# Optimization experiments

Measured on AMD Instinct MI355X. Metric: run time of the kernel, lower is better.

The kernel has to match this reference:

```python
import jax, jax.numpy as jnp
import numpy as np

N = 200_000          # instances (patches) in the bag
D = 512              # dim_compress_features
NCLS = 2             # n_class
NINS = 8             # n_ins (top-k per polarity)


def setup_inputs() -> dict:
    key = jax.random.key(0)
    k1, k2, k3 = jax.random.split(key, 3)
    return {
        "bag_label": 1,
        "h": jax.random.normal(k1, (N, D), dtype=jnp.float32),
        "A": jax.random.normal(k2, (N, 1, NCLS), dtype=jnp.float32),
        # Dense(n_class) params of the (shared) instance classifier
        "W": jax.random.normal(k3, (D, NCLS), dtype=jnp.float32) * 0.02,
        "b": jnp.zeros((NCLS,), dtype=jnp.float32),
    }


def reference(bag_label, h, A, W, b):
    # Attention scores for the bag's class: A[j][0][bag_label]  -> [N]
    A_I = A[:, 0, bag_label]
    # top n_ins most-attended (positive evidence) and least-attended (negative)
    _, pos_idx = jax.lax.top_k(A_I, NINS)    # [NINS]
    _, neg_idx = jax.lax.top_k(-A_I, NINS)   # [NINS]
    idx = jnp.concatenate([pos_idx, neg_idx], axis=0)   # [2*NINS]
    ins_in = h[idx]                                      # gather -> [2*NINS, D]
    # Batched Dense + softmax (replaces the per-instance Python loop)
    logits_unnorm = ins_in @ W + b                       # [2*NINS, NCLS]
    logits = jax.nn.softmax(logits_unnorm, axis=-1)      # [2*NINS, NCLS]
    ins_labels = jnp.concatenate(
        [jnp.full((NINS,), 1, dtype=jnp.int32), jnp.full((NINS,), 0, dtype=jnp.int32)]
    )
    return ins_labels, logits_unnorm, logits
```

## Files before the change

kernel.cpp:

```cpp
#include <hip/hip_runtime.h>
#include <math.h>

#define N_ELEMS 200000
#define D 512
#define NCLS 2
#define NINS 8
#define NBLK1 128
#define NTHR1 512
#define NTHR2 1024

typedef unsigned long long u64;
typedef unsigned int u32;

__device__ __forceinline__ u32 mono(float f) {
    u32 u = __float_as_uint(f);
    return u ^ (u32)(((int)u >> 31) | 0x80000000);
}

__device__ __forceinline__ u64 make_key(float v, int i) {
    return ((u64)mono(v) << 32) | (u32)(~(u32)i);
}
__device__ __forceinline__ int key_idx(u64 k) { return (int)(~(u32)k); }

__device__ __forceinline__ u64 shfl_xor_u64(u64 x, int m) {
    u32 lo = (u32)x, hi = (u32)(x >> 32);
    lo = __shfl_xor(lo, m, 64);
    hi = __shfl_xor(hi, m, 64);
    return ((u64)hi << 32) | lo;
}

__device__ __forceinline__ u64 wave_max_u64(u64 k) {
#pragma unroll
    for (int m = 1; m < 64; m <<= 1) {
        u64 o = shfl_xor_u64(k, m);
        if (o > k) k = o;
    }
    return k;
}

__global__ __launch_bounds__(NTHR1) void scan_partial(const int* __restrict__ bl_ptr,
                                                      const float* __restrict__ A,
                                                      u64* __restrict__ wsTop,
                                                      u64* __restrict__ wsBot) {
    const int tid  = threadIdx.x;
    const int blk  = blockIdx.x;
    const int wid  = tid >> 6;
    const int lane = tid & 63;
    const int bl   = bl_ptr[0];

    __shared__ u64 cand[2][8][NINS];

    const int chunk = (N_ELEMS + NBLK1 - 1) / NBLK1;
    const int start = blk * chunk;
    const int end   = min(N_ELEMS, start + chunk);
    const float2* A2 = (const float2*)A;

    u64 t0, t1, t2, t3, b0, b1, b2, b3;
    {
        int i0 = start + tid, i1 = i0 + NTHR1, i2 = i1 + NTHR1, i3 = i2 + NTHR1;
        float2 a;
        if (i0 < end) { a = A2[i0]; float v = bl ? a.y : a.x; t0 = make_key(v, i0); b0 = make_key(-v, i0); } else { t0 = b0 = 0; }
        if (i1 < end) { a = A2[i1]; float v = bl ? a.y : a.x; t1 = make_key(v, i1); b1 = make_key(-v, i1); } else { t1 = b1 = 0; }
        if (i2 < end) { a = A2[i2]; float v = bl ? a.y : a.x; t2 = make_key(v, i2); b2 = make_key(-v, i2); } else { t2 = b2 = 0; }
        if (i3 < end) { a = A2[i3]; float v = bl ? a.y : a.x; t3 = make_key(v, i3); b3 = make_key(-v, i3); } else { t3 = b3 = 0; }
    }

#pragma unroll
    for (int r = 0; r < NINS; ++r) {
        u64 m01 = t0 > t1 ? t0 : t1;
        u64 m23 = t2 > t3 ? t2 : t3;
        u64 lm  = m01 > m23 ? m01 : m23;
        u64 w   = wave_max_u64(lm);
        if (lane == 0) cand[0][wid][r] = w;
        if (t0 == w) t0 = 0; if (t1 == w) t1 = 0; if (t2 == w) t2 = 0; if (t3 == w) t3 = 0;
    }
#pragma unroll
    for (int r = 0; r < NINS; ++r) {
        u64 m01 = b0 > b1 ? b0 : b1;
        u64 m23 = b2 > b3 ? b2 : b3;
        u64 lm  = m01 > m23 ? m01 : m23;
        u64 w   = wave_max_u64(lm);
        if (lane == 0) cand[1][wid][r] = w;
        if (b0 == w) b0 = 0; if (b1 == w) b1 = 0; if (b2 == w) b2 = 0; if (b3 == w) b3 = 0;
    }
    __syncthreads();

    if (wid < 2) {
        u64 k = cand[wid][lane >> 3][lane & 7];
        u64 mine = 0;
#pragma unroll
        for (int r = 0; r < NINS; ++r) {
            u64 w = wave_max_u64(k);
            if (lane == r) mine = w;
            if (k == w) k = 0;
        }
        u64* dst = (wid == 0) ? wsTop : wsBot;
        if (lane < NINS) dst[blk * NINS + lane] = mine;
    }
}

__global__ __launch_bounds__(NTHR2) void finalize(const float* __restrict__ h,
                                                  const float* __restrict__ W,
                                                  const float* __restrict__ bvec,
                                                  const u64* __restrict__ wsTop,
                                                  const u64* __restrict__ wsBot,
                                                  float* __restrict__ out) {
    const int tid  = threadIdx.x;
    const int wid  = tid >> 6;
    const int lane = tid & 63;

    __shared__ u64 cand2[16][NINS];
    __shared__ int fidx[2 * NINS];

    {
        const u64* src = (wid < 8) ? wsTop : wsBot;
        const int base = (wid & 7) * 128;
        u64 ka = src[base + lane];
        u64 kb = src[base + 64 + lane];
        u64 mine = 0;
#pragma unroll
        for (int r = 0; r < NINS; ++r) {
            u64 m_ = ka > kb ? ka : kb;
            u64 w  = wave_max_u64(m_);
            if (lane == r) mine = w;
            if (ka == w) ka = 0;
            if (kb == w) kb = 0;
        }
        if (lane < NINS) cand2[wid][lane] = mine;
    }
    __syncthreads();

    if ((wid & 7) == 0) {
        const u64* flat = &cand2[(wid >> 3) * 8][0];
        u64 k = flat[lane];
        int got = 0;
#pragma unroll
        for (int r = 0; r < NINS; ++r) {
            u64 w = wave_max_u64(k);
            if (lane == r) got = key_idx(w);
            if (k == w) k = 0;
        }
        if (lane < NINS) fidx[(wid >> 3) * NINS + lane] = got;
    }
    __syncthreads();

    const long long row = fidx[wid];
    const float4* h4 = (const float4*)(h + row * (long long)D);
    const float2* W2 = (const float2*)W;

    float s0 = 0.f, s1 = 0.f;
#pragma unroll
    for (int it = 0; it < 2; ++it) {
        int d4 = lane + it * 64;
        float4 x = h4[d4];
        float2 w0 = W2[d4 * 4 + 0];
        float2 w1 = W2[d4 * 4 + 1];
        float2 w2 = W2[d4 * 4 + 2];
        float2 w3 = W2[d4 * 4 + 3];
        s0 += x.x * w0.x + x.y * w1.x + x.z * w2.x + x.w * w3.x;
        s1 += x.x * w0.y + x.y * w1.y + x.z * w2.y + x.w * w3.y;
    }
#pragma unroll
    for (int m = 1; m < 64; m <<= 1) {
        s0 += __shfl_xor(s0, m, 64);
        s1 += __shfl_xor(s1, m, 64);
    }
    if (lane == 0) {
        float l0 = s0 + bvec[0];
        float l1 = s1 + bvec[1];
        float mx = fmaxf(l0, l1);
        float e0 = expf(l0 - mx), e1 = expf(l1 - mx);
        float inv = 1.0f / (e0 + e1);
        out[16 + wid * 2 + 0] = l0;
        out[16 + wid * 2 + 1] = l1;
        out[48 + wid * 2 + 0] = e0 * inv;
        out[48 + wid * 2 + 1] = e1 * inv;
    }
    if (tid < 16) out[tid] = (tid < 8) ? 1.0f : 0.0f;
}

extern "C" void kernel_launch(void* const* d_in, const int* in_sizes, int n_in,
                              void* d_out, int out_size, void* d_ws, size_t ws_size,
                              hipStream_t stream) {
    const int*   bl = (const int*)  d_in[0];
    const float* h  = (const float*)d_in[1];
    const float* A  = (const float*)d_in[2];
    const float* W  = (const float*)d_in[3];
    const float* b  = (const float*)d_in[4];
    float* out = (float*)d_out;

    char* ws = (char*)d_ws;
    u64* wsTop = (u64*)(ws + 0);
    u64* wsBot = (u64*)(ws + 8192);

    scan_partial<<<NBLK1, NTHR1, 0, stream>>>(bl, A, wsTop, wsBot);
    finalize<<<1, NTHR2, 0, stream>>>(h, W, b, wsTop, wsBot, out);
}
```

Baseline: 25.27 us.

## Fuse scan and finalize into one cooperative kernel with grid sync

Merges the partial top-k scan and the final reduction/gather/dense into a single cooperative kernel that uses a grid-wide barrier instead of a second kernel launch. The finalize phase is reworked for 512 threads: each wave reduces four candidates per lane and computes two output rows. This targets the launch gap between the two small kernels, but cooperative launch plus grid sync carries its own overhead. If cooperative launch fails, it falls back to the two-kernel path.

```diff
diff --git a/kernel.cpp b/kernel.cpp
--- a/kernel.cpp
+++ b/kernel.cpp
@@ -1,13 +1,15 @@
 #include <hip/hip_runtime.h>
+#include <hip/hip_cooperative_groups.h>
 #include <math.h>
+
+namespace cg = cooperative_groups;
 
 #define N_ELEMS 200000
 #define D 512
 #define NCLS 2
 #define NINS 8
-#define NBLK1 128
-#define NTHR1 512
-#define NTHR2 1024
+#define NBLK 128
+#define NTHR 512
 
 typedef unsigned long long u64;
 typedef unsigned int u32;
@@ -38,26 +40,18 @@
     return k;
 }
 
-__global__ __launch_bounds__(NTHR1) void scan_partial(const int* __restrict__ bl_ptr,
-                                                      const float* __restrict__ A,
-                                                      u64* __restrict__ wsTop,
-                                                      u64* __restrict__ wsBot) {
-    const int tid  = threadIdx.x;
-    const int blk  = blockIdx.x;
-    const int wid  = tid >> 6;
-    const int lane = tid & 63;
-    const int bl   = bl_ptr[0];
-
-    __shared__ u64 cand[2][8][NINS];
-
-    const int chunk = (N_ELEMS + NBLK1 - 1) / NBLK1;
+__device__ __forceinline__ void scan_phase(int blk, int tid, int wid, int lane, int bl,
+                                           const float* __restrict__ A,
+                                           u64* __restrict__ wsTop, u64* __restrict__ wsBot,
+                                           u64 (*cand)[8][NINS]) {
+    const int chunk = (N_ELEMS + NBLK - 1) / NBLK;
     const int start = blk * chunk;
     const int end   = min(N_ELEMS, start + chunk);
     const float2* A2 = (const float2*)A;
 
     u64 t0, t1, t2, t3, b0, b1, b2, b3;
     {
-        int i0 = start + tid, i1 = i0 + NTHR1, i2 = i1 + NTHR1, i3 = i2 + NTHR1;
+        int i0 = start + tid, i1 = i0 + NTHR, i2 = i1 + NTHR, i3 = i2 + NTHR;
         float2 a;
         if (i0 < end) { a = A2[i0]; float v = bl ? a.y : a.x; t0 = make_key(v, i0); b0 = make_key(-v, i0); } else { t0 = b0 = 0; }
         if (i1 < end) { a = A2[i1]; float v = bl ? a.y : a.x; t1 = make_key(v, i1); b1 = make_key(-v, i1); } else { t1 = b1 = 0; }
@@ -99,40 +93,34 @@
     }
 }
 
-__global__ __launch_bounds__(NTHR2) void finalize(const float* __restrict__ h,
-                                                  const float* __restrict__ W,
-                                                  const float* __restrict__ bvec,
-                                                  const u64* __restrict__ wsTop,
-                                                  const u64* __restrict__ wsBot,
-                                                  float* __restrict__ out) {
-    const int tid  = threadIdx.x;
-    const int wid  = tid >> 6;
-    const int lane = tid & 63;
-
-    __shared__ u64 cand2[16][NINS];
-    __shared__ int fidx[2 * NINS];
-
+__device__ __forceinline__ void final_phase(int tid, int wid, int lane,
+                                            const float* __restrict__ h,
+                                            const float* __restrict__ W,
+                                            const float* __restrict__ bvec,
+                                            const u64* __restrict__ wsTop,
+                                            const u64* __restrict__ wsBot,
+                                            float* __restrict__ out,
+                                            u64 (*cand2)[NINS], int* fidx) {
     {
-        const u64* src = (wid < 8) ? wsTop : wsBot;
-        const int base = (wid & 7) * 128;
-        u64 ka = src[base + lane];
-        u64 kb = src[base + 64 + lane];
+        const u64* src = (wid < 4) ? wsTop : wsBot;
+        const int base = (wid & 3) * 256 + lane;
+        u64 k0 = src[base], k1 = src[base + 64], k2 = src[base + 128], k3 = src[base + 192];
         u64 mine = 0;
 #pragma unroll
         for (int r = 0; r < NINS; ++r) {
-            u64 m_ = ka > kb ? ka : kb;
-            u64 w  = wave_max_u64(m_);
+            u64 m01 = k0 > k1 ? k0 : k1;
+            u64 m23 = k2 > k3 ? k2 : k3;
+            u64 lm  = m01 > m23 ? m01 : m23;
+            u64 w   = wave_max_u64(lm);
             if (lane == r) mine = w;
-            if (ka == w) ka = 0;
-            if (kb == w) kb = 0;
+            if (k0 == w) k0 = 0; if (k1 == w) k1 = 0; if (k2 == w) k2 = 0; if (k3 == w) k3 = 0;
         }
         if (lane < NINS) cand2[wid][lane] = mine;
     }
     __syncthreads();
 
-    if ((wid & 7) == 0) {
-        const u64* flat = &cand2[(wid >> 3) * 8][0];
-        u64 k = flat[lane];
+    if ((wid & 3) == 0) {
+        u64 k = (lane < 32) ? cand2[(wid & 4) + (lane >> 3)][lane & 7] : 0ULL;
         int got = 0;
 #pragma unroll
         for (int r = 0; r < NINS; ++r) {
@@ -140,43 +128,91 @@
             if (lane == r) got = key_idx(w);
             if (k == w) k = 0;
         }
-        if (lane < NINS) fidx[(wid >> 3) * NINS + lane] = got;
+        if (lane < NINS) fidx[(wid >> 2) * NINS + lane] = got;
     }
     __syncthreads();
 
-    const long long row = fidx[wid];
-    const float4* h4 = (const float4*)(h + row * (long long)D);
     const float2* W2 = (const float2*)W;
-
-    float s0 = 0.f, s1 = 0.f;
-#pragma unroll
-    for (int it = 0; it < 2; ++it) {
-        int d4 = lane + it * 64;
-        float4 x = h4[d4];
-        float2 w0 = W2[d4 * 4 + 0];
-        float2 w1 = W2[d4 * 4 + 1];
-        float2 w2 = W2[d4 * 4 + 2];
-        float2 w3 = W2[d4 * 4 + 3];
-        s0 += x.x * w0.x + x.y * w1.x + x.z * w2.x + x.w * w3.x;
-        s1 += x.x * w0.y + x.y * w1.y + x.z * w2.y + x.w * w3.y;
-    }
-#pragma unroll
-    for (int m = 1; m < 64; m <<= 1) {
-        s0 += __shfl_xor(s0, m, 64);
-        s1 += __shfl_xor(s1, m, 64);
-    }
-    if (lane == 0) {
-        float l0 = s0 + bvec[0];
-        float l1 = s1 + bvec[1];
-        float mx = fmaxf(l0, l1);
-        float e0 = expf(l0 - mx), e1 = expf(l1 - mx);
-        float inv = 1.0f / (e0 + e1);
-        out[16 + wid * 2 + 0] = l0;
-        out[16 + wid * 2 + 1] = l1;
-        out[48 + wid * 2 + 0] = e0 * inv;
-        out[48 + wid * 2 + 1] = e1 * inv;
+#pragma unroll
+    for (int rr = 0; rr < 2; ++rr) {
+        const int g = wid + rr * 8;
+        const long long row = fidx[g];
+        const float4* h4 = (const float4*)(h + row * (long long)D);
+        float s0 = 0.f, s1 = 0.f;
+#pragma unroll
+        for (int it = 0; it < 2; ++it) {
+            int d4 = lane + it * 64;
+            float4 x = h4[d4];
+            float2 w0 = W2[d4 * 4 + 0];
+            float2 w1 = W2[d4 * 4 + 1];
+            float2 w2 = W2[d4 * 4 + 2];
+            float2 w3 = W2[d4 * 4 + 3];
+            s0 += x.x * w0.x + x.y * w1.x + x.z * w2.x + x.w * w3.x;
+            s1 += x.x * w0.y + x.y * w1.y + x.z * w2.y + x.w * w3.y;
+        }
+#pragma unroll
+        for (int m = 1; m < 64; m <<= 1) {
+            s0 += __shfl_xor(s0, m, 64);
+            s1 += __shfl_xor(s1, m, 64);
+        }
+        if (lane == 0) {
+            float l0 = s0 + bvec[0];
+            float l1 = s1 + bvec[1];
+            float mx = fmaxf(l0, l1);
+            float e0 = expf(l0 - mx), e1 = expf(l1 - mx);
+            float inv = 1.0f / (e0 + e1);
+            out[16 + g * 2 + 0] = l0;
+            out[16 + g * 2 + 1] = l1;
+            out[48 + g * 2 + 0] = e0 * inv;
+            out[48 + g * 2 + 1] = e1 * inv;
+        }
     }
     if (tid < 16) out[tid] = (tid < 8) ? 1.0f : 0.0f;
+}
+
+__global__ __launch_bounds__(NTHR) void ins_coop(const int* __restrict__ bl_ptr,
+                                                 const float* __restrict__ A,
+                                                 const float* __restrict__ h,
+                                                 const float* __restrict__ W,
+                                                 const float* __restrict__ bvec,
+                                                 u64* __restrict__ wsTop,
+                                                 u64* __restrict__ wsBot,
+                                                 float* __restrict__ out) {
+    const int tid  = threadIdx.x;
+    const int wid  = tid >> 6;
+    const int lane = tid & 63;
+
+    __shared__ u64 cand[2][8][NINS];
+    __shared__ u64 cand2[8][NINS];
+    __shared__ int fidx[16];
+
+    scan_phase(blockIdx.x, tid, wid, lane, bl_ptr[0], A, wsTop, wsBot, cand);
+
+    cg::this_grid().sync();
+    if (blockIdx.x != 0) return;
+
+    final_phase(tid, wid, lane, h, W, bvec, wsTop, wsBot, out, cand2, fidx);
+}
+
+__global__ __launch_bounds__(NTHR) void scan_partial(const int* __restrict__ bl_ptr,
+                                                     const float* __restrict__ A,
+                                                     u64* __restrict__ wsTop,
+                                                     u64* __restrict__ wsBot) {
+    __shared__ u64 cand[2][8][NINS];
+    scan_phase(blockIdx.x, threadIdx.x, threadIdx.x >> 6, threadIdx.x & 63,
+               bl_ptr[0], A, wsTop, wsBot, cand);
+}
+
+__global__ __launch_bounds__(NTHR) void finalize(const float* __restrict__ h,
+                                                 const float* __restrict__ W,
+                                                 const float* __restrict__ bvec,
+                                                 const u64* __restrict__ wsTop,
+                                                 const u64* __restrict__ wsBot,
+                                                 float* __restrict__ out) {
+    __shared__ u64 cand2[8][NINS];
+    __shared__ int fidx[16];
+    final_phase(threadIdx.x, threadIdx.x >> 6, threadIdx.x & 63,
+                h, W, bvec, wsTop, wsBot, out, cand2, fidx);
 }
 
 extern "C" void kernel_launch(void* const* d_in, const int* in_sizes, int n_in,
@@ -193,6 +229,12 @@
     u64* wsTop = (u64*)(ws + 0);
     u64* wsBot = (u64*)(ws + 8192);
 
-    scan_partial<<<NBLK1, NTHR1, 0, stream>>>(bl, A, wsTop, wsBot);
-    finalize<<<1, NTHR2, 0, stream>>>(h, W, b, wsTop, wsBot, out);
-}
+    void* args[] = { (void*)&bl, (void*)&A, (void*)&h, (void*)&W, (void*)&b,
+                     (void*)&wsTop, (void*)&wsBot, (void*)&out };
+    hipError_t e = hipLaunchCooperativeKernel(reinterpret_cast<void*>(ins_coop),
+                                              dim3(NBLK), dim3(NTHR), args, 0, stream);
+    if (e != hipSuccess) {
+        scan_partial<<<NBLK, NTHR, 0, stream>>>(bl, A, wsTop, wsBot);
+        finalize<<<1, NTHR, 0, stream>>>(h, W, b, wsTop, wsBot, out);
+    }
+}
```

Measured after the change: 52.82 us. 109% more time.
